# Performance work log

Measured on AMD Instinct MI355X. Metric: run time of the kernel, lower is better.

## Reference

```python
import jax, jax.numpy as jnp
import numpy as np

B, S, H = 2, 2048, 3584
NH, NKV, HD = 28, 4, 128
GROUPS = NH // NKV  # 7
SCALING = HD ** -0.5
NEG = -1e9


def setup_inputs() -> dict:
    key = jax.random.key(0)
    ks = jax.random.split(key, 10)
    hidden_states = jax.random.normal(ks[0], (B, S, H), jnp.float32)
    # RoPE tables (faithful functional form; use real rotary angles)
    inv_freq = 1.0 / (1000000.0 ** (jnp.arange(0, HD, 2, dtype=jnp.float32) / HD))
    pos = jnp.arange(S, dtype=jnp.float32)
    freqs = jnp.outer(pos, inv_freq)                 # [S, HD/2]
    emb = jnp.concatenate([freqs, freqs], axis=-1)   # [S, HD]
    cos = jnp.broadcast_to(jnp.cos(emb)[None], (B, S, HD))
    sin = jnp.broadcast_to(jnp.sin(emb)[None], (B, S, HD))
    # additive causal mask [1,1,S,S]
    causal = jnp.tril(jnp.ones((S, S), dtype=bool))
    attention_mask = jnp.where(causal, 0.0, NEG).astype(jnp.float32)[None, None]
    sc = 0.02
    Wq = jax.random.normal(ks[1], (NH * HD, H), jnp.float32) * sc
    bq = jax.random.normal(ks[2], (NH * HD,), jnp.float32) * sc
    Wk = jax.random.normal(ks[3], (NKV * HD, H), jnp.float32) * sc
    bk = jax.random.normal(ks[4], (NKV * HD,), jnp.float32) * sc
    Wv = jax.random.normal(ks[5], (NKV * HD, H), jnp.float32) * sc
    bv = jax.random.normal(ks[6], (NKV * HD,), jnp.float32) * sc
    Wo = jax.random.normal(ks[7], (H, NH * HD), jnp.float32) * sc
    return dict(hidden_states=hidden_states, cos=cos, sin=sin,
                attention_mask=attention_mask, Wq=Wq, bq=bq, Wk=Wk, bk=bk,
                Wv=Wv, bv=bv, Wo=Wo)


def _rotate_half(x):
    x1, x2 = jnp.split(x, 2, axis=-1)
    return jnp.concatenate([-x2, x1], axis=-1)


def reference(hidden_states, cos, sin, attention_mask, Wq, bq, Wk, bk, Wv, bv, Wo):
    Bv_, Sv_ = hidden_states.shape[:2]
    # projections -> [B, heads, S, HD]
    q = (hidden_states @ Wq.T + bq).reshape(Bv_, Sv_, NH, HD).transpose(0, 2, 1, 3)
    k = (hidden_states @ Wk.T + bk).reshape(Bv_, Sv_, NKV, HD).transpose(0, 2, 1, 3)
    v = (hidden_states @ Wv.T + bv).reshape(Bv_, Sv_, NKV, HD).transpose(0, 2, 1, 3)
    # RoPE (unsqueeze_dim=1)
    c, s = cos[:, None], sin[:, None]
    q = q * c + _rotate_half(q) * s
    k = k * c + _rotate_half(k) * s
    # repeat_kv for GQA
    k = jnp.repeat(k, GROUPS, axis=1)  # [B, NH, S, HD]
    v = jnp.repeat(v, GROUPS, axis=1)
    scores = jnp.einsum('bhqd,bhkd->bhqk', q, k) * SCALING
    scores = scores + attention_mask[:, :, :, :k.shape[-2]]
    probs = jax.nn.softmax(scores.astype(jnp.float32), axis=-1).astype(q.dtype)
    attn = jnp.einsum('bhqk,bhkd->bhqd', probs, v)          # [B, NH, S, HD]
    attn = attn.transpose(0, 2, 1, 3).reshape(Bv_, Sv_, NH * HD)
    out = attn @ Wo.T
    return out, probs
```

## Files before the change

### kernel.cpp

```cpp
#include <hip/hip_runtime.h>

#define Bn 2
#define Sn 2048
#define Hn 3584
#define NHn 28
#define NKVn 4
#define HDn 128
#define GROUPSn 7
#define SCALEF 0.08838834764831845f
#define NOUT 14680064LL

typedef __attribute__((ext_vector_type(4))) float f4v;
typedef __attribute__((ext_vector_type(16))) float f32x16;
typedef __attribute__((ext_vector_type(8))) short bf16x8;
typedef __attribute__((ext_vector_type(4))) short s16x4;

typedef __attribute__((address_space(1))) void gvoid;
typedef __attribute__((address_space(3))) void lvoid;
#define GLL16(g, l) __builtin_amdgcn_global_load_lds((gvoid*)(void*)(g), (lvoid*)(l), 16, 0, 0)

__device__ __forceinline__ short f2bf(float f) {
  unsigned u = __builtin_bit_cast(unsigned, f);
  u = (u + 0x7fffu + ((u >> 16) & 1u)) >> 16;
  return (short)u;
}

__global__ __launch_bounds__(256) void cast_bf16(const float* __restrict__ in,
                                                 short* __restrict__ out, long long n4) {
  long long i = (long long)blockIdx.x * 256 + threadIdx.x;
  long long stride = (long long)gridDim.x * 256;
  for (; i < n4; i += stride) {
    f4v f = ((const f4v*)in)[i];
    s16x4 o = { f2bf(f.x), f2bf(f.y), f2bf(f.z), f2bf(f.w) };
    ((s16x4*)out)[i] = o;
  }
}

__global__ __launch_bounds__(256) void concat_bias(const float* __restrict__ bq,
                                                   const float* __restrict__ bk,
                                                   const float* __restrict__ bv,
                                                   float* __restrict__ out) {
  int i = blockIdx.x * 256 + threadIdx.x;
  if (i < 3584) out[i] = bq[i];
  else if (i < 4096) out[i] = bk[i - 3584];
  else if (i < 4608) out[i] = bv[i - 4096];
}

__device__ __forceinline__ void mm128_core(const short* __restrict__ Atile, long long lda,
                                           const short* __restrict__ Btile, long long ldb,
                                           int nk, short* lA, short* lB, f4v (&acc)[4][4]) {
  const int tid = threadIdx.x;
  const int lane = tid & 63;
  const int wr = (tid >> 6) >> 1, wc = (tid >> 6) & 1;
  const int srow = tid >> 2;
  const int scol = (tid & 3) * 8;
  const short* a0 = Atile + (long long)srow * lda + scol;
  const short* a1 = Atile + (long long)(srow + 64) * lda + scol;
  const short* b0 = Btile + (long long)srow * ldb + scol;
  const short* b1 = Btile + (long long)(srow + 64) * ldb + scol;
  short* la0 = lA + tid * 8;
  short* la1 = lA + (256 + tid) * 8;
  short* lb0 = lB + tid * 8;
  short* lb1 = lB + (256 + tid) * 8;
  const int fr = lane & 15;
  const int kc = (lane >> 4) * 8;
  for (int kt = 0; kt < nk; ++kt) {
    GLL16(a0 + kt * 32, la0);
    GLL16(a1 + kt * 32, la1);
    GLL16(b0 + kt * 32, lb0);
    GLL16(b1 + kt * 32, lb1);
    __syncthreads();
    bf16x8 af[4], bf[4];
#pragma unroll
    for (int m = 0; m < 4; ++m)
      af[m] = *(const bf16x8*)&lA[(wr * 64 + m * 16 + fr) * 32 + kc];
#pragma unroll
    for (int n = 0; n < 4; ++n)
      bf[n] = *(const bf16x8*)&lB[(wc * 64 + n * 16 + fr) * 32 + kc];
#pragma unroll
    for (int m = 0; m < 4; ++m)
#pragma unroll
      for (int n = 0; n < 4; ++n)
        acc[m][n] = __builtin_amdgcn_mfma_f32_16x16x32_bf16(af[m], bf[n], acc[m][n], 0, 0, 0);
    __syncthreads();
  }
}

__global__ __launch_bounds__(256) void gemm_bias_f32(const short* __restrict__ A,
                                                     const short* __restrict__ B,
                                                     float* __restrict__ C,
                                                     const float* __restrict__ bias,
                                                     int K, int N) {
  __shared__ alignas(16) short lA[4096];
  __shared__ alignas(16) short lB[4096];
  const long long brow = (long long)blockIdx.y * 128;
  const long long bcol = (long long)blockIdx.x * 128;
  f4v acc[4][4] = {};
  mm128_core(A + brow * K, K, B + bcol * K, K, K >> 5, lA, lB, acc);
  const int lane = threadIdx.x & 63;
  const int wr = (threadIdx.x >> 6) >> 1, wc = (threadIdx.x >> 6) & 1;
  const int rr = (lane >> 4) * 4, cc = lane & 15;
#pragma unroll
  for (int n = 0; n < 4; ++n) {
    long long col = bcol + wc * 64 + n * 16 + cc;
    float bv = bias ? bias[col] : 0.f;
#pragma unroll
    for (int m = 0; m < 4; ++m) {
#pragma unroll
      for (int j = 0; j < 4; ++j) {
        long long row = brow + wr * 64 + m * 16 + rr + j;
        C[row * N + col] = acc[m][n][j] + bv;
      }
    }
  }
}

__global__ __launch_bounds__(256) void rope_qk(const float* __restrict__ qkv,
                                               const float* __restrict__ cosb,
                                               const float* __restrict__ sinb,
                                               short* __restrict__ qo,
                                               short* __restrict__ ko) {
  long long bs = blockIdx.x;
  int b = (int)(bs >> 11);
  int s = (int)(bs & 2047);
  const float* row = qkv + bs * 4608;
  const float* cp = cosb + bs * 128;
  const float* sp = sinb + bs * 128;
  for (int i = threadIdx.x; i < 4096; i += 256) {
    int d = i & 127;
    float c = cp[d], sn = sp[d];
    float x = row[i];
    float xr = (d < 64) ? -row[i + 64] : row[i - 64];
    short v = f2bf(x * c + xr * sn);
    if (i < 3584) {
      int h = i >> 7;
      qo[(((long long)(b * NHn + h) * Sn + s)) * HDn + d] = v;
    } else {
      int h = (i - 3584) >> 7;
      ko[(((long long)(b * NKVn + h) * Sn + s)) * HDn + d] = v;
    }
  }
}

__global__ void vtrans(const float* __restrict__ qkv, short* __restrict__ vt) {
  __shared__ float tile[32][33];
  int bh = blockIdx.z;
  int b = bh >> 2, h = bh & 3;
  int s0 = blockIdx.x * 32, d0 = blockIdx.y * 32;
  int tx = threadIdx.x, ty = threadIdx.y;
#pragma unroll
  for (int j = 0; j < 32; j += 8) {
    int s = s0 + ty + j;
    tile[ty + j][tx] = qkv[((long long)(b * Sn + s)) * 4608 + 4096 + h * 128 + d0 + tx];
  }
  __syncthreads();
#pragma unroll
  for (int j = 0; j < 32; j += 8) {
    int d = d0 + ty + j;
    vt[((long long)(bh * 128 + d)) * Sn + s0 + tx] = f2bf(tile[tx][ty + j]);
  }
}

__global__ __launch_bounds__(256) void zero_upper(float* probs) {
  int ck = blockIdx.x, qb = blockIdx.y, bh = blockIdx.z;
  if (ck <= qb) return;
  float* base = probs + (long long)bh * ((long long)Sn * Sn) +
                (long long)qb * 128 * Sn + (long long)ck * 128;
  int tid = threadIdx.x;
  int r0 = tid >> 3;
  int c0 = tid & 7;
  f4v z = {0.f, 0.f, 0.f, 0.f};
  for (int rr = 0; rr < 128; rr += 32) {
    f4v* rowp = (f4v*)(base + (long long)(r0 + rr) * Sn);
#pragma unroll
    for (int c = 0; c < 4; ++c) __builtin_nontemporal_store(z, &rowp[c0 + c * 8]);
  }
}

__global__ __launch_bounds__(256, 2) void fused_attn2(const short* __restrict__ Q,
                                                      const short* __restrict__ Kb,
                                                      const short* __restrict__ Vt,
                                                      float* __restrict__ probs,
                                                      short* __restrict__ attn) {
  __shared__ alignas(16) short lK[2][16384];
  const int tid = threadIdx.x;
  const int w = tid >> 6;
  const int lane = tid & 63;
  const int lam = lane & 31, h = lane >> 5;
  const int qb = 15 - (int)blockIdx.x;
  const int bh = blockIdx.y;
  const int b = bh / NHn, hh = bh - b * NHn, kv = hh / GROUPSn;
  const short* Qb = Q + (long long)bh * (Sn * HDn);
  const short* Kbb = Kb + (long long)(b * NKVn + kv) * (Sn * HDn);
  const short* Vb = Vt + (long long)(b * NKVn + kv) * (HDn * Sn);
  float* Pb = probs + (long long)bh * ((long long)Sn * Sn) + (long long)qb * 128 * Sn;
  const int qloc = w * 32 + lam;

  bf16x8 qf[8];
  {
    const short* qr = Qb + (long long)(qb * 128 + qloc) * HDn + h * 8;
#pragma unroll
    for (int s = 0; s < 8; ++s) qf[s] = *(const bf16x8*)(qr + s * 16);
  }
  int rsw[8], csw[8];
#pragma unroll
  for (int i = 0; i < 8; ++i) {
    int M = i * 256 + tid;
    rsw[i] = M >> 4;
    csw[i] = (M & 15) ^ (rsw[i] & 15);
  }
  const int c8base = lam & 15;
  const int nkt = qb + 1;

#define STAGEK(BUF, KT) do {                                                      \
    const short* base_ = Kbb + (long long)(KT) * 128 * HDn;                       \
    _Pragma("unroll")                                                             \
    for (int i = 0; i < 8; ++i)                                                   \
      GLL16(base_ + (long long)rsw[i] * HDn + csw[i] * 8,                         \
            (short*)lK[BUF] + (i * 256 + tid) * 8);                               \
  } while (0)

#define QKT(ACCP, LCUR) do {                                                      \
    _Pragma("unroll")                                                             \
    for (int s = 0; s < 8; ++s) {                                                 \
      const int co_ = ((s * 2 + h) ^ c8base) * 8;                                 \
      _Pragma("unroll")                                                           \
      for (int a = 0; a < 4; ++a) {                                               \
        bf16x8 kf_ = *(const bf16x8*)&(LCUR)[(a * 32 + lam) * 128 + co_];         \
        ACCP[a] = __builtin_amdgcn_mfma_f32_32x32x16_bf16(kf_, qf[s], ACCP[a], 0, 0, 0); \
      }                                                                           \
    }                                                                             \
  } while (0)

  float lsum = 0.f;
  STAGEK(0, 0);
  int cur = 0;
  for (int kt = 0; kt < nkt; ++kt) {
    __syncthreads();
    if (kt + 1 < nkt) STAGEK(cur ^ 1, kt + 1);
    const short* lcur = (const short*)lK[cur];
    f32x16 accp[4] = {};
    QKT(accp, lcur);
    const bool diag = (kt == qb);
#pragma unroll
    for (int a = 0; a < 4; ++a)
#pragma unroll
      for (int r = 0; r < 16; ++r) {
        int kloc = a * 32 + (r & 3) + 8 * (r >> 2) + 4 * h;
        float s = fminf(accp[a][r] * SCALEF, 60.f);
        float p = __expf(s);
        if (diag && kloc > qloc) p = 0.f;
        lsum += p;
      }
    cur ^= 1;
  }
  lsum += __shfl_xor(lsum, 32);
  const float invl = 1.f / lsum;

  __syncthreads();
  STAGEK(0, 0);
  cur = 0;
  f32x16 acco[4] = {};
  for (int kt = 0; kt < nkt; ++kt) {
    __syncthreads();
    if (kt + 1 < nkt) STAGEK(cur ^ 1, kt + 1);
    const short* lcur = (const short*)lK[cur];
    f32x16 accp[4] = {};
    QKT(accp, lcur);
    const bool diag = (kt == qb);
    float* prow = Pb + (long long)qloc * Sn + kt * 128 + 4 * h;
    const short* vrow = Vb + (long long)lam * Sn + kt * 128 + h * 8;
#pragma unroll
    for (int a = 0; a < 4; ++a) {
      float pn[16];
#pragma unroll
      for (int r = 0; r < 16; ++r) {
        int kloc = a * 32 + (r & 3) + 8 * (r >> 2) + 4 * h;
        float s = fminf(accp[a][r] * SCALEF, 60.f);
        float p = __expf(s) * invl;
        if (diag && kloc > qloc) p = 0.f;
        pn[r] = p;
      }
#pragma unroll
      for (int T = 0; T < 4; ++T) {
        f4v v = { pn[4 * T], pn[4 * T + 1], pn[4 * T + 2], pn[4 * T + 3] };
        *(f4v*)(prow + a * 32 + 8 * T) = v;
      }
#pragma unroll
      for (int ci = 0; ci < 2; ++ci) {
        const int ro = ci * 8;
        float r0 = __shfl_xor(h ? pn[ro + 0] : pn[ro + 4], 32);
        float r1 = __shfl_xor(h ? pn[ro + 1] : pn[ro + 5], 32);
        float r2 = __shfl_xor(h ? pn[ro + 2] : pn[ro + 6], 32);
        float r3 = __shfl_xor(h ? pn[ro + 3] : pn[ro + 7], 32);
        float t0 = h ? r0 : pn[ro + 0];
        float t1 = h ? r1 : pn[ro + 1];
        float t2 = h ? r2 : pn[ro + 2];
        float t3 = h ? r3 : pn[ro + 3];
        float t4 = h ? pn[ro + 4] : r0;
        float t5 = h ? pn[ro + 5] : r1;
        float t6 = h ? pn[ro + 6] : r2;
        float t7 = h ? pn[ro + 7] : r3;
        bf16x8 pf = { f2bf(t0), f2bf(t1), f2bf(t2), f2bf(t3),
                      f2bf(t4), f2bf(t5), f2bf(t6), f2bf(t7) };
        const int c = a * 2 + ci;
#pragma unroll
        for (int f = 0; f < 4; ++f) {
          bf16x8 vf = *(const bf16x8*)(vrow + (long long)f * 32 * Sn + c * 16);
          acco[f] = __builtin_amdgcn_mfma_f32_32x32x16_bf16(pf, vf, acco[f], 0, 0, 0);
        }
      }
    }
    cur ^= 1;
  }
#undef QKT
#undef STAGEK

#pragma unroll
  for (int f = 0; f < 4; ++f)
#pragma unroll
    for (int r = 0; r < 16; ++r) {
      int qv = (r & 3) + 8 * (r >> 2) + 4 * h;
      long long q = (long long)qb * 128 + w * 32 + qv;
      attn[((long long)(b * Sn) + q) * Hn + hh * HDn + f * 32 + lam] = f2bf(acco[f][r]);
    }
}


extern "C" void kernel_launch(void* const* d_in, const int* in_sizes, int n_in,
                              void* d_out, int out_size, void* d_ws, size_t ws_size,
                              hipStream_t stream) {
  const float* hs   = (const float*)d_in[0];
  const float* cosb = (const float*)d_in[1];
  const float* sinb = (const float*)d_in[2];
  const float* Wq = (const float*)d_in[4];
  const float* bq = (const float*)d_in[5];
  const float* Wk = (const float*)d_in[6];
  const float* bk = (const float*)d_in[7];
  const float* Wv = (const float*)d_in[8];
  const float* bv = (const float*)d_in[9];
  const float* Wo = (const float*)d_in[10];
  float* out   = (float*)d_out;
  float* probs = out + NOUT;
  char* ws = (char*)d_ws;
  short* hs_bf   = (short*)(ws + 0);
  short* attn_bf = hs_bf;
  short* wqkv_bf = (short*)(ws + 29360128LL);
  short* q_bf    = wqkv_bf;
  short* wo_bf   = (short*)(ws + 62390272LL);
  float* bias_qkv= (float*)(ws + 88080384LL);
  float* qkv     = (float*)(ws + 88098816LL);
  short* k_bf    = (short*)(ws + 163596288LL);
  short* vt_bf   = (short*)(ws + 167790592LL);

  cast_bf16<<<2048, 256, 0, stream>>>(hs, hs_bf, 3670016LL);
  cast_bf16<<<2048, 256, 0, stream>>>(Wq, wqkv_bf, 3211264LL);
  cast_bf16<<<512, 256, 0, stream>>>(Wk, wqkv_bf + 12845056LL, 458752LL);
  cast_bf16<<<512, 256, 0, stream>>>(Wv, wqkv_bf + 14680064LL, 458752LL);
  cast_bf16<<<2048, 256, 0, stream>>>(Wo, wo_bf, 3211264LL);
  concat_bias<<<18, 256, 0, stream>>>(bq, bk, bv, bias_qkv);

  gemm_bias_f32<<<dim3(36, 32), 256, 0, stream>>>(hs_bf, wqkv_bf, qkv, bias_qkv, 3584, 4608);

  rope_qk<<<4096, 256, 0, stream>>>(qkv, cosb, sinb, q_bf, k_bf);
  vtrans<<<dim3(64, 4, 8), dim3(32, 8), 0, stream>>>(qkv, vt_bf);

  zero_upper<<<dim3(16, 16, 56), 256, 0, stream>>>(probs);
  fused_attn2<<<dim3(16, 56), 256, 0, stream>>>(q_bf, k_bf, vt_bf, probs, attn_bf);

  gemm_bias_f32<<<dim3(28, 32), 256, 0, stream>>>(attn_bf, wo_bf, out, nullptr, 3584, 3584);
}
```

Measured before the change: 1.078 ms.

## Swizzle GEMM blocks across XCDs, split attention QK^T pass, nontemporal prob stores

```diff
diff --git a/kernel.cpp b/kernel.cpp
--- a/kernel.cpp
+++ b/kernel.cpp
@@ -90,11 +90,16 @@
                                                      const short* __restrict__ B,
                                                      float* __restrict__ C,
                                                      const float* __restrict__ bias,
-                                                     int K, int N) {
+                                                     int K, int N, int gx) {
   __shared__ alignas(16) short lA[4096];
   __shared__ alignas(16) short lB[4096];
-  const long long brow = (long long)blockIdx.y * 128;
-  const long long bcol = (long long)blockIdx.x * 128;
+  int nwg = gridDim.x * gridDim.y;
+  int bid = (int)blockIdx.y * gridDim.x + (int)blockIdx.x;
+  int cpx = nwg >> 3;
+  int swz = (bid & 7) * cpx + (bid >> 3);
+  int bx = swz % gx, by = swz / gx;
+  const long long brow = (long long)by * 128;
+  const long long bcol = (long long)bx * 128;
   f4v acc[4][4] = {};
   mm128_core(A + brow * K, K, B + bcol * K, K, K >> 5, lA, lB, acc);
   const int lane = threadIdx.x & 63;
@@ -177,7 +182,7 @@
   }
 }
 
-__global__ __launch_bounds__(256, 2) void fused_attn2(const short* __restrict__ Q,
+__global__ __launch_bounds__(256, 1) void fused_attn2(const short* __restrict__ Q,
                                                       const short* __restrict__ Kb,
                                                       const short* __restrict__ Vt,
                                                       float* __restrict__ probs,
@@ -220,18 +225,6 @@
             (short*)lK[BUF] + (i * 256 + tid) * 8);                               \
   } while (0)
 
-#define QKT(ACCP, LCUR) do {                                                      \
-    _Pragma("unroll")                                                             \
-    for (int s = 0; s < 8; ++s) {                                                 \
-      const int co_ = ((s * 2 + h) ^ c8base) * 8;                                 \
-      _Pragma("unroll")                                                           \
-      for (int a = 0; a < 4; ++a) {                                               \
-        bf16x8 kf_ = *(const bf16x8*)&(LCUR)[(a * 32 + lam) * 128 + co_];         \
-        ACCP[a] = __builtin_amdgcn_mfma_f32_32x32x16_bf16(kf_, qf[s], ACCP[a], 0, 0, 0); \
-      }                                                                           \
-    }                                                                             \
-  } while (0)
-
   float lsum = 0.f;
   STAGEK(0, 0);
   int cur = 0;
@@ -240,7 +233,15 @@
     if (kt + 1 < nkt) STAGEK(cur ^ 1, kt + 1);
     const short* lcur = (const short*)lK[cur];
     f32x16 accp[4] = {};
-    QKT(accp, lcur);
+#pragma unroll
+    for (int s = 0; s < 8; ++s) {
+      const int co_ = ((s * 2 + h) ^ c8base) * 8;
+#pragma unroll
+      for (int a = 0; a < 4; ++a) {
+        bf16x8 kf_ = *(const bf16x8*)&lcur[(a * 32 + lam) * 128 + co_];
+        accp[a] = __builtin_amdgcn_mfma_f32_32x32x16_bf16(kf_, qf[s], accp[a], 0, 0, 0);
+      }
+    }
     const bool diag = (kt == qb);
 #pragma unroll
     for (int a = 0; a < 4; ++a)
@@ -265,55 +266,67 @@
     __syncthreads();
     if (kt + 1 < nkt) STAGEK(cur ^ 1, kt + 1);
     const short* lcur = (const short*)lK[cur];
-    f32x16 accp[4] = {};
-    QKT(accp, lcur);
     const bool diag = (kt == qb);
     float* prow = Pb + (long long)qloc * Sn + kt * 128 + 4 * h;
     const short* vrow = Vb + (long long)lam * Sn + kt * 128 + h * 8;
 #pragma unroll
-    for (int a = 0; a < 4; ++a) {
-      float pn[16];
-#pragma unroll
-      for (int r = 0; r < 16; ++r) {
-        int kloc = a * 32 + (r & 3) + 8 * (r >> 2) + 4 * h;
-        float s = fminf(accp[a][r] * SCALEF, 60.f);
-        float p = __expf(s) * invl;
-        if (diag && kloc > qloc) p = 0.f;
-        pn[r] = p;
-      }
-#pragma unroll
-      for (int T = 0; T < 4; ++T) {
-        f4v v = { pn[4 * T], pn[4 * T + 1], pn[4 * T + 2], pn[4 * T + 3] };
-        *(f4v*)(prow + a * 32 + 8 * T) = v;
-      }
-#pragma unroll
-      for (int ci = 0; ci < 2; ++ci) {
-        const int ro = ci * 8;
-        float r0 = __shfl_xor(h ? pn[ro + 0] : pn[ro + 4], 32);
-        float r1 = __shfl_xor(h ? pn[ro + 1] : pn[ro + 5], 32);
-        float r2 = __shfl_xor(h ? pn[ro + 2] : pn[ro + 6], 32);
-        float r3 = __shfl_xor(h ? pn[ro + 3] : pn[ro + 7], 32);
-        float t0 = h ? r0 : pn[ro + 0];
-        float t1 = h ? r1 : pn[ro + 1];
-        float t2 = h ? r2 : pn[ro + 2];
-        float t3 = h ? r3 : pn[ro + 3];
-        float t4 = h ? pn[ro + 4] : r0;
-        float t5 = h ? pn[ro + 5] : r1;
-        float t6 = h ? pn[ro + 6] : r2;
-        float t7 = h ? pn[ro + 7] : r3;
-        bf16x8 pf = { f2bf(t0), f2bf(t1), f2bf(t2), f2bf(t3),
-                      f2bf(t4), f2bf(t5), f2bf(t6), f2bf(t7) };
-        const int c = a * 2 + ci;
-#pragma unroll
-        for (int f = 0; f < 4; ++f) {
-          bf16x8 vf = *(const bf16x8*)(vrow + (long long)f * 32 * Sn + c * 16);
-          acco[f] = __builtin_amdgcn_mfma_f32_32x32x16_bf16(pf, vf, acco[f], 0, 0, 0);
+    for (int ap = 0; ap < 2; ++ap) {
+      f32x16 accp[2] = {};
+#pragma unroll
+      for (int s = 0; s < 8; ++s) {
+        const int co_ = ((s * 2 + h) ^ c8base) * 8;
+#pragma unroll
+        for (int aa = 0; aa < 2; ++aa) {
+          const int a = ap * 2 + aa;
+          bf16x8 kf_ = *(const bf16x8*)&lcur[(a * 32 + lam) * 128 + co_];
+          accp[aa] = __builtin_amdgcn_mfma_f32_32x32x16_bf16(kf_, qf[s], accp[aa], 0, 0, 0);
         }
       }
+#pragma unroll
+      for (int aa = 0; aa < 2; ++aa) {
+        const int a = ap * 2 + aa;
+        float pn[16];
+#pragma unroll
+        for (int r = 0; r < 16; ++r) {
+          int kloc = a * 32 + (r & 3) + 8 * (r >> 2) + 4 * h;
+          float s = fminf(accp[aa][r] * SCALEF, 60.f);
+          float p = __expf(s) * invl;
+          if (diag && kloc > qloc) p = 0.f;
+          pn[r] = p;
+        }
+#pragma unroll
+        for (int T = 0; T < 4; ++T) {
+          f4v v = { pn[4 * T], pn[4 * T + 1], pn[4 * T + 2], pn[4 * T + 3] };
+          __builtin_nontemporal_store(v, (f4v*)(prow + a * 32 + 8 * T));
+        }
+#pragma unroll
+        for (int ci = 0; ci < 2; ++ci) {
+          const int ro = ci * 8;
+          float r0 = __shfl_xor(h ? pn[ro + 0] : pn[ro + 4], 32);
+          float r1 = __shfl_xor(h ? pn[ro + 1] : pn[ro + 5], 32);
+          float r2 = __shfl_xor(h ? pn[ro + 2] : pn[ro + 6], 32);
+          float r3 = __shfl_xor(h ? pn[ro + 3] : pn[ro + 7], 32);
+          float t0 = h ? r0 : pn[ro + 0];
+          float t1 = h ? r1 : pn[ro + 1];
+          float t2 = h ? r2 : pn[ro + 2];
+          float t3 = h ? r3 : pn[ro + 3];
+          float t4 = h ? pn[ro + 4] : r0;
+          float t5 = h ? pn[ro + 5] : r1;
+          float t6 = h ? pn[ro + 6] : r2;
+          float t7 = h ? pn[ro + 7] : r3;
+          bf16x8 pf = { f2bf(t0), f2bf(t1), f2bf(t2), f2bf(t3),
+                        f2bf(t4), f2bf(t5), f2bf(t6), f2bf(t7) };
+          const int c = a * 2 + ci;
+#pragma unroll
+          for (int f = 0; f < 4; ++f) {
+            bf16x8 vf = *(const bf16x8*)(vrow + (long long)f * 32 * Sn + c * 16);
+            acco[f] = __builtin_amdgcn_mfma_f32_32x32x16_bf16(pf, vf, acco[f], 0, 0, 0);
+          }
+        }
+      }
     }
     cur ^= 1;
   }
-#undef QKT
 #undef STAGEK
 
 #pragma unroll
@@ -360,7 +373,7 @@
   cast_bf16<<<2048, 256, 0, stream>>>(Wo, wo_bf, 3211264LL);
   concat_bias<<<18, 256, 0, stream>>>(bq, bk, bv, bias_qkv);
 
-  gemm_bias_f32<<<dim3(36, 32), 256, 0, stream>>>(hs_bf, wqkv_bf, qkv, bias_qkv, 3584, 4608);
+  gemm_bias_f32<<<dim3(36, 32), 256, 0, stream>>>(hs_bf, wqkv_bf, qkv, bias_qkv, 3584, 4608, 36);
 
   rope_qk<<<4096, 256, 0, stream>>>(qkv, cosb, sinb, q_bf, k_bf);
   vtrans<<<dim3(64, 4, 8), dim3(32, 8), 0, stream>>>(qkv, vt_bf);
@@ -368,5 +381,5 @@
   zero_upper<<<dim3(16, 16, 56), 256, 0, stream>>>(probs);
   fused_attn2<<<dim3(16, 56), 256, 0, stream>>>(q_bf, k_bf, vt_bf, probs, attn_bf);
 
-  gemm_bias_f32<<<dim3(28, 32), 256, 0, stream>>>(attn_bf, wo_bf, out, nullptr, 3584, 3584);
-}
+  gemm_bias_f32<<<dim3(28, 32), 256, 0, stream>>>(attn_bf, wo_bf, out, nullptr, 3584, 3584, 28);
+}
```

After: 1.242 ms. +15.2%, slower.
